# Kernel tuning notes

Hardware: AMD Instinct MI355X
Metric: run time of the kernel (lower is better)

Reference implementation:

```python
import jax, jax.numpy as jnp
import numpy as np

K, N, V_DIM, H_DIM, G_DIM, U_DIM = 8, 100000, 128, 128, 64, 128
W_SCALE = 0.1  # ~ xavier_uniform std for these fan-in/fan-out sizes


def setup_inputs() -> dict:
    key = jax.random.key(0)
    k1, k2, k3, k4, k5 = jax.random.split(key, 5)
    return {
        "vt": jax.random.normal(k1, (N, V_DIM), dtype=jnp.float32),
        "H": jax.random.normal(k2, (K, N, H_DIM), dtype=jnp.float32),
        "Wgv": jax.random.normal(k3, (V_DIM, G_DIM), dtype=jnp.float32) * W_SCALE,
        "Wgh": jax.random.normal(k4, (K, H_DIM, G_DIM), dtype=jnp.float32) * W_SCALE,
        "Wuh": jax.random.normal(k5, (K, H_DIM, U_DIM), dtype=jnp.float32) * W_SCALE,
    }


def reference(vt, H, Wgv, Wgh, Wuh):
    lrelu = lambda x: jnp.where(x >= 0, x, 0.01 * x)  # nn.LeakyReLU default slope
    g_key = vt @ Wgv                                   # [N, g]
    g_query = jnp.einsum("knh,khg->kng", H, Wgh)       # [k, N, g]
    g = jnp.einsum("kng,ng->kn", g_query, g_key)       # [k, N]
    g = jnp.exp(lrelu(g) / jnp.sqrt(jnp.float32(G_DIM)))
    beta = g / jnp.sum(g, axis=0, keepdims=True)       # normalize over k per node
    H_trans = jnp.einsum("knh,khu->knu", H, Wuh)       # [k, N, u]
    U = jnp.einsum("kn,knu->nu", beta, H_trans)        # [N, u]
    return lrelu(U)
```

## Files before the change

kernel.cpp:

```cpp
#include <hip/hip_runtime.h>
#include <stdint.h>

#define KH 8
#define HD 128
#define GD 64
#define UD 128
#define WPAD 136
#define NPB 64

typedef __attribute__((ext_vector_type(8))) short short8;
typedef __attribute__((ext_vector_type(4))) float f32x4;

__device__ __forceinline__ unsigned short f2bf(float x) {
    union { float f; unsigned u; } v; v.f = x;
    return (unsigned short)((v.u + 0x7fffu + ((v.u >> 16) & 1u)) >> 16);
}

__global__ void prep_weights(const float* __restrict__ Wgv,
                             const float* __restrict__ Wgh,
                             const float* __restrict__ Wuh,
                             unsigned short* __restrict__ ws) {
    const int wghN = KH * GD * WPAD;
    const int wuhN = KH * UD * WPAD;
    const int wgvN = GD * WPAD;
    int idx = blockIdx.x * 256 + threadIdx.x;
    if (idx >= wghN + wuhN + wgvN) return;
    float val = 0.f;
    if (idx < wghN) {
        int k = idx / (GD * WPAD), rem = idx % (GD * WPAD);
        int g = rem / WPAD, h = rem % WPAD;
        if (h < HD) val = Wgh[((size_t)k * HD + h) * GD + g];
    } else if (idx < wghN + wuhN) {
        int j = idx - wghN;
        int k = j / (UD * WPAD), rem = j % (UD * WPAD);
        int u = rem / WPAD, h = rem % WPAD;
        if (h < HD) val = Wuh[((size_t)k * HD + h) * UD + u];
    } else {
        int j = idx - wghN - wuhN;
        int g = j / WPAD, h = j % WPAD;
        if (h < HD) val = Wgv[(size_t)h * GD + g];
    }
    ws[idx] = f2bf(val);
}

__device__ __forceinline__ void cp_lds(const unsigned short* gs, unsigned short* ld,
                                       int nch, int wave, int lane) {
    for (int i = wave; i < nch; i += 4) {
        __builtin_amdgcn_global_load_lds(
            (const __attribute__((address_space(1))) unsigned int*)(gs + i * 512 + lane * 8),
            (__attribute__((address_space(3))) unsigned int*)(ld + i * 512),
            16, 0, 0);
    }
}

__launch_bounds__(256, 3)
__global__ void ghatt_main(const float* __restrict__ vt, const float* __restrict__ H,
                           const unsigned short* __restrict__ ws,
                           float* __restrict__ out, int N) {
    __shared__ unsigned short lds_h [NPB * WPAD];
    __shared__ unsigned short lds_wg[GD * WPAD];
    __shared__ unsigned short lds_wu[GD * WPAD];

    const int tid  = threadIdx.x;
    const int wave = tid >> 6;
    const int lane = tid & 63;
    const int cc   = lane & 15;
    const int q    = lane >> 4;
    const int nodebase = blockIdx.x * NPB;

    const unsigned short* wghT = ws;
    const unsigned short* wuhT = ws + (size_t)KH * GD * WPAD;
    const unsigned short* wgvT = ws + (size_t)KH * GD * WPAD + (size_t)KH * UD * WPAD;

    float4 hreg[8];

#pragma unroll
    for (int i = 0; i < 8; i++) {
        int f = tid + 256 * i, row = f >> 5, c4 = f & 31;
        int node = nodebase + row;
        float4 z; z.x = z.y = z.z = z.w = 0.f;
        float4 v = (node < N) ? ((const float4*)vt)[(size_t)node * 32 + c4] : z;
        short4 b;
        b.x = (short)f2bf(v.x); b.y = (short)f2bf(v.y);
        b.z = (short)f2bf(v.z); b.w = (short)f2bf(v.w);
        *(short4*)&lds_h[row * WPAD + c4 * 4] = b;
    }
    cp_lds(wgvT, lds_wg, 17, wave, lane);
    __syncthreads();

#pragma unroll
    for (int i = 0; i < 8; i++) {
        int f = tid + 256 * i, row = f >> 5, c4 = f & 31;
        int node = nodebase + row;
        float4 z; z.x = z.y = z.z = z.w = 0.f;
        hreg[i] = (node < N) ? ((const float4*)H)[(size_t)node * 32 + c4] : z;
    }

    f32x4 gkeyv[4];
    {
        short8 va[4];
#pragma unroll
        for (int kb = 0; kb < 4; kb++)
            va[kb] = *(const short8*)&lds_h[(wave * 16 + cc) * WPAD + kb * 32 + q * 8];
#pragma unroll
        for (int t = 0; t < 4; t++) {
            f32x4 acc = {0.f, 0.f, 0.f, 0.f};
#pragma unroll
            for (int kb = 0; kb < 4; kb++) {
                short8 vb = *(const short8*)&lds_wg[(t * 16 + cc) * WPAD + kb * 32 + q * 8];
                acc = __builtin_amdgcn_mfma_f32_16x16x32_bf16(va[kb], vb, acc, 0, 0, 0);
            }
            gkeyv[t] = acc;
        }
    }

    f32x4 Uacc[8];
#pragma unroll
    for (int t = 0; t < 8; t++) { Uacc[t].x = Uacc[t].y = Uacc[t].z = Uacc[t].w = 0.f; }
    float den[4] = {0.f, 0.f, 0.f, 0.f};

    for (int k = 0; k < KH; k++) {
        __syncthreads();
#pragma unroll
        for (int i = 0; i < 8; i++) {
            int f = tid + 256 * i, row = f >> 5, c4 = f & 31;
            short4 b;
            b.x = (short)f2bf(hreg[i].x); b.y = (short)f2bf(hreg[i].y);
            b.z = (short)f2bf(hreg[i].z); b.w = (short)f2bf(hreg[i].w);
            *(short4*)&lds_h[row * WPAD + c4 * 4] = b;
        }
        cp_lds(wghT + (size_t)k * (GD * WPAD), lds_wg, 17, wave, lane);
        cp_lds(wuhT + (size_t)k * (UD * WPAD), lds_wu, 17, wave, lane);
        __syncthreads();

        if (k < KH - 1) {
#pragma unroll
            for (int i = 0; i < 8; i++) {
                int f = tid + 256 * i, row = f >> 5, c4 = f & 31;
                int node = nodebase + row;
                float4 z; z.x = z.y = z.z = z.w = 0.f;
                hreg[i] = (node < N) ? ((const float4*)H)[((size_t)(k + 1) * N + node) * 32 + c4] : z;
            }
        }

        short8 va[4];
#pragma unroll
        for (int kb = 0; kb < 4; kb++)
            va[kb] = *(const short8*)&lds_h[(wave * 16 + cc) * WPAD + kb * 32 + q * 8];

        f32x4 gqv[4];
#pragma unroll
        for (int t = 0; t < 4; t++) {
            f32x4 acc = {0.f, 0.f, 0.f, 0.f};
#pragma unroll
            for (int kb = 0; kb < 4; kb++) {
                short8 vb = *(const short8*)&lds_wg[(t * 16 + cc) * WPAD + kb * 32 + q * 8];
                acc = __builtin_amdgcn_mfma_f32_16x16x32_bf16(va[kb], vb, acc, 0, 0, 0);
            }
            gqv[t] = acc;
        }

        float part[4];
#pragma unroll
        for (int r = 0; r < 4; r++)
            part[r] = gqv[0][r] * gkeyv[0][r] + gqv[1][r] * gkeyv[1][r]
                    + gqv[2][r] * gkeyv[2][r] + gqv[3][r] * gkeyv[3][r];
#pragma unroll
        for (int m2 = 1; m2 < 16; m2 <<= 1) {
#pragma unroll
            for (int r = 0; r < 4; r++) part[r] += __shfl_xor(part[r], m2);
        }
        float gg[4];
#pragma unroll
        for (int r = 0; r < 4; r++) {
            float x = part[r];
            x = (x >= 0.f) ? x : 0.01f * x;
            gg[r] = __expf(x * 0.125f);
            den[r] += gg[r];
        }

#pragma unroll
        for (int t = 0; t < 4; t++) {
            f32x4 acc = {0.f, 0.f, 0.f, 0.f};
#pragma unroll
            for (int kb = 0; kb < 4; kb++) {
                short8 vb = *(const short8*)&lds_wu[(t * 16 + cc) * WPAD + kb * 32 + q * 8];
                acc = __builtin_amdgcn_mfma_f32_16x16x32_bf16(va[kb], vb, acc, 0, 0, 0);
            }
#pragma unroll
            for (int r = 0; r < 4; r++) Uacc[t][r] += gg[r] * acc[r];
        }

        __syncthreads();
        cp_lds(wuhT + (size_t)k * (UD * WPAD) + (size_t)64 * WPAD, lds_wu, 17, wave, lane);
        __syncthreads();

#pragma unroll
        for (int t = 0; t < 4; t++) {
            f32x4 acc = {0.f, 0.f, 0.f, 0.f};
#pragma unroll
            for (int kb = 0; kb < 4; kb++) {
                short8 vb = *(const short8*)&lds_wu[(t * 16 + cc) * WPAD + kb * 32 + q * 8];
                acc = __builtin_amdgcn_mfma_f32_16x16x32_bf16(va[kb], vb, acc, 0, 0, 0);
            }
#pragma unroll
            for (int r = 0; r < 4; r++) Uacc[4 + t][r] += gg[r] * acc[r];
        }
    }

    float inv[4];
#pragma unroll
    for (int r = 0; r < 4; r++) inv[r] = 1.f / den[r];
#pragma unroll
    for (int t = 0; t < 8; t++) {
#pragma unroll
        for (int r = 0; r < 4; r++) {
            float u = Uacc[t][r] * inv[r];
            u = (u >= 0.f) ? u : 0.01f * u;
            int node = nodebase + wave * 16 + 4 * q + r;
            if (node < N) out[(size_t)node * UD + t * 16 + cc] = u;
        }
    }
}

extern "C" void kernel_launch(void* const* d_in, const int* in_sizes, int n_in,
                              void* d_out, int out_size, void* d_ws, size_t ws_size,
                              hipStream_t stream) {
    const float* vt  = (const float*)d_in[0];
    const float* H   = (const float*)d_in[1];
    const float* Wgv = (const float*)d_in[2];
    const float* Wgh = (const float*)d_in[3];
    const float* Wuh = (const float*)d_in[4];
    float* out = (float*)d_out;
    unsigned short* wsw = (unsigned short*)d_ws;

    const int N = in_sizes[0] / HD;

    const int prepTot = KH * GD * WPAD + KH * UD * WPAD + GD * WPAD;
    hipLaunchKernelGGL(prep_weights, dim3((prepTot + 255) / 256), dim3(256), 0, stream,
                       Wgv, Wgh, Wuh, wsw);

    hipLaunchKernelGGL(ghatt_main, dim3((N + NPB - 1) / NPB), dim3(256), 0, stream,
                       vt, H, wsw, out, N);
}
```

Before: 669.9 us.

## Drop LDS staging; load H rows and bf16 weights straight into MFMA registers

New measurement: 851.9 us. +27.2%, slower.

```diff
diff --git a/kernel.cpp b/kernel.cpp
--- a/kernel.cpp
+++ b/kernel.cpp
@@ -5,7 +5,6 @@
 #define HD 128
 #define GD 64
 #define UD 128
-#define WPAD 136
 #define NPB 64
 
 typedef __attribute__((ext_vector_type(8))) short short8;
@@ -20,151 +19,133 @@
                              const float* __restrict__ Wgh,
                              const float* __restrict__ Wuh,
                              unsigned short* __restrict__ ws) {
-    const int wghN = KH * GD * WPAD;
-    const int wuhN = KH * UD * WPAD;
-    const int wgvN = GD * WPAD;
+    const int wghN = KH * GD * HD;
+    const int wuhN = KH * UD * HD;
+    const int wgvN = GD * HD;
     int idx = blockIdx.x * 256 + threadIdx.x;
     if (idx >= wghN + wuhN + wgvN) return;
-    float val = 0.f;
+    float val;
     if (idx < wghN) {
-        int k = idx / (GD * WPAD), rem = idx % (GD * WPAD);
-        int g = rem / WPAD, h = rem % WPAD;
-        if (h < HD) val = Wgh[((size_t)k * HD + h) * GD + g];
+        int k = idx >> 13, rem = idx & 8191;
+        int g = rem >> 7, h = rem & 127;
+        val = Wgh[((size_t)k * HD + h) * GD + g];
     } else if (idx < wghN + wuhN) {
         int j = idx - wghN;
-        int k = j / (UD * WPAD), rem = j % (UD * WPAD);
-        int u = rem / WPAD, h = rem % WPAD;
-        if (h < HD) val = Wuh[((size_t)k * HD + h) * UD + u];
+        int k = j >> 14, rem = j & 16383;
+        int u = rem >> 7, h = rem & 127;
+        val = Wuh[((size_t)k * HD + h) * UD + u];
     } else {
         int j = idx - wghN - wuhN;
-        int g = j / WPAD, h = j % WPAD;
-        if (h < HD) val = Wgv[(size_t)h * GD + g];
+        int g = j >> 7, h = j & 127;
+        val = Wgv[(size_t)h * GD + g];
     }
     ws[idx] = f2bf(val);
-}
-
-__device__ __forceinline__ void cp_lds(const unsigned short* gs, unsigned short* ld,
-                                       int nch, int wave, int lane) {
-    for (int i = wave; i < nch; i += 4) {
-        __builtin_amdgcn_global_load_lds(
-            (const __attribute__((address_space(1))) unsigned int*)(gs + i * 512 + lane * 8),
-            (__attribute__((address_space(3))) unsigned int*)(ld + i * 512),
-            16, 0, 0);
-    }
 }
 
 __launch_bounds__(256, 3)
 __global__ void ghatt_main(const float* __restrict__ vt, const float* __restrict__ H,
                            const unsigned short* __restrict__ ws,
                            float* __restrict__ out, int N) {
-    __shared__ unsigned short lds_h [NPB * WPAD];
-    __shared__ unsigned short lds_wg[GD * WPAD];
-    __shared__ unsigned short lds_wu[GD * WPAD];
-
     const int tid  = threadIdx.x;
     const int wave = tid >> 6;
     const int lane = tid & 63;
     const int cc   = lane & 15;
     const int q    = lane >> 4;
-    const int nodebase = blockIdx.x * NPB;
+    const int nodebase = blockIdx.x * NPB + wave * 16;
+    const int node_a   = nodebase + cc;
+    const int nm       = node_a < N ? node_a : N - 1;
 
     const unsigned short* wghT = ws;
-    const unsigned short* wuhT = ws + (size_t)KH * GD * WPAD;
-    const unsigned short* wgvT = ws + (size_t)KH * GD * WPAD + (size_t)KH * UD * WPAD;
+    const unsigned short* wuhT = ws + (size_t)KH * GD * HD;
+    const unsigned short* wgvT = ws + (size_t)KH * GD * HD + (size_t)KH * UD * HD;
 
     float4 hreg[8];
-
-#pragma unroll
-    for (int i = 0; i < 8; i++) {
-        int f = tid + 256 * i, row = f >> 5, c4 = f & 31;
-        int node = nodebase + row;
-        float4 z; z.x = z.y = z.z = z.w = 0.f;
-        float4 v = (node < N) ? ((const float4*)vt)[(size_t)node * 32 + c4] : z;
-        short4 b;
-        b.x = (short)f2bf(v.x); b.y = (short)f2bf(v.y);
-        b.z = (short)f2bf(v.z); b.w = (short)f2bf(v.w);
-        *(short4*)&lds_h[row * WPAD + c4 * 4] = b;
-    }
-    cp_lds(wgvT, lds_wg, 17, wave, lane);
-    __syncthreads();
-
-#pragma unroll
-    for (int i = 0; i < 8; i++) {
-        int f = tid + 256 * i, row = f >> 5, c4 = f & 31;
-        int node = nodebase + row;
-        float4 z; z.x = z.y = z.z = z.w = 0.f;
-        hreg[i] = (node < N) ? ((const float4*)H)[(size_t)node * 32 + c4] : z;
-    }
-
-    f32x4 gkeyv[4];
+    short8 ha[4];
+
     {
-        short8 va[4];
-#pragma unroll
-        for (int kb = 0; kb < 4; kb++)
-            va[kb] = *(const short8*)&lds_h[(wave * 16 + cc) * WPAD + kb * 32 + q * 8];
+        const float* vrow = vt + (size_t)nm * HD + q * 8;
+#pragma unroll
+        for (int kb = 0; kb < 4; kb++) {
+            hreg[2 * kb]     = *(const float4*)(vrow + kb * 32);
+            hreg[2 * kb + 1] = *(const float4*)(vrow + kb * 32 + 4);
+        }
+#pragma unroll
+        for (int kb = 0; kb < 4; kb++) {
+            const float* p0 = (const float*)&hreg[2 * kb];
+            const float* p1 = (const float*)&hreg[2 * kb + 1];
+            short8 s;
+#pragma unroll
+            for (int j = 0; j < 4; j++) {
+                s[j]     = (short)f2bf(p0[j]);
+                s[4 + j] = (short)f2bf(p1[j]);
+            }
+            ha[kb] = s;
+        }
+    }
+    f32x4 gkey[4];
+#pragma unroll
+    for (int t = 0; t < 4; t++) {
+        f32x4 acc = {0.f, 0.f, 0.f, 0.f};
+#pragma unroll
+        for (int kb = 0; kb < 4; kb++) {
+            short8 wb = *(const short8*)(wgvT + (size_t)(t * 16 + cc) * HD + kb * 32 + q * 8);
+            acc = __builtin_amdgcn_mfma_f32_16x16x32_bf16(ha[kb], wb, acc, 0, 0, 0);
+        }
+        gkey[t] = acc;
+    }
+
+    f32x4 Uacc[8];
+#pragma unroll
+    for (int t = 0; t < 8; t++) { Uacc[t].x = Uacc[t].y = Uacc[t].z = Uacc[t].w = 0.f; }
+    float den[4] = {0.f, 0.f, 0.f, 0.f};
+
+    const float* hrow = H + (size_t)nm * HD + q * 8;
+#pragma unroll
+    for (int kb = 0; kb < 4; kb++) {
+        hreg[2 * kb]     = *(const float4*)(hrow + kb * 32);
+        hreg[2 * kb + 1] = *(const float4*)(hrow + kb * 32 + 4);
+    }
+
+    for (int k = 0; k < KH; k++) {
+#pragma unroll
+        for (int kb = 0; kb < 4; kb++) {
+            const float* p0 = (const float*)&hreg[2 * kb];
+            const float* p1 = (const float*)&hreg[2 * kb + 1];
+            short8 s;
+#pragma unroll
+            for (int j = 0; j < 4; j++) {
+                s[j]     = (short)f2bf(p0[j]);
+                s[4 + j] = (short)f2bf(p1[j]);
+            }
+            ha[kb] = s;
+        }
+        if (k < KH - 1) {
+            const float* hn = hrow + (size_t)(k + 1) * N * HD;
+#pragma unroll
+            for (int kb = 0; kb < 4; kb++) {
+                hreg[2 * kb]     = *(const float4*)(hn + kb * 32);
+                hreg[2 * kb + 1] = *(const float4*)(hn + kb * 32 + 4);
+            }
+        }
+
+        const unsigned short* wg = wghT + (size_t)k * GD * HD;
+        f32x4 gq[4];
 #pragma unroll
         for (int t = 0; t < 4; t++) {
             f32x4 acc = {0.f, 0.f, 0.f, 0.f};
 #pragma unroll
             for (int kb = 0; kb < 4; kb++) {
-                short8 vb = *(const short8*)&lds_wg[(t * 16 + cc) * WPAD + kb * 32 + q * 8];
-                acc = __builtin_amdgcn_mfma_f32_16x16x32_bf16(va[kb], vb, acc, 0, 0, 0);
-            }
-            gkeyv[t] = acc;
-        }
-    }
-
-    f32x4 Uacc[8];
-#pragma unroll
-    for (int t = 0; t < 8; t++) { Uacc[t].x = Uacc[t].y = Uacc[t].z = Uacc[t].w = 0.f; }
-    float den[4] = {0.f, 0.f, 0.f, 0.f};
-
-    for (int k = 0; k < KH; k++) {
-        __syncthreads();
-#pragma unroll
-        for (int i = 0; i < 8; i++) {
-            int f = tid + 256 * i, row = f >> 5, c4 = f & 31;
-            short4 b;
-            b.x = (short)f2bf(hreg[i].x); b.y = (short)f2bf(hreg[i].y);
-            b.z = (short)f2bf(hreg[i].z); b.w = (short)f2bf(hreg[i].w);
-            *(short4*)&lds_h[row * WPAD + c4 * 4] = b;
-        }
-        cp_lds(wghT + (size_t)k * (GD * WPAD), lds_wg, 17, wave, lane);
-        cp_lds(wuhT + (size_t)k * (UD * WPAD), lds_wu, 17, wave, lane);
-        __syncthreads();
-
-        if (k < KH - 1) {
-#pragma unroll
-            for (int i = 0; i < 8; i++) {
-                int f = tid + 256 * i, row = f >> 5, c4 = f & 31;
-                int node = nodebase + row;
-                float4 z; z.x = z.y = z.z = z.w = 0.f;
-                hreg[i] = (node < N) ? ((const float4*)H)[((size_t)(k + 1) * N + node) * 32 + c4] : z;
-            }
-        }
-
-        short8 va[4];
-#pragma unroll
-        for (int kb = 0; kb < 4; kb++)
-            va[kb] = *(const short8*)&lds_h[(wave * 16 + cc) * WPAD + kb * 32 + q * 8];
-
-        f32x4 gqv[4];
-#pragma unroll
-        for (int t = 0; t < 4; t++) {
-            f32x4 acc = {0.f, 0.f, 0.f, 0.f};
-#pragma unroll
-            for (int kb = 0; kb < 4; kb++) {
-                short8 vb = *(const short8*)&lds_wg[(t * 16 + cc) * WPAD + kb * 32 + q * 8];
-                acc = __builtin_amdgcn_mfma_f32_16x16x32_bf16(va[kb], vb, acc, 0, 0, 0);
-            }
-            gqv[t] = acc;
+                short8 wb = *(const short8*)(wg + (size_t)(t * 16 + cc) * HD + kb * 32 + q * 8);
+                acc = __builtin_amdgcn_mfma_f32_16x16x32_bf16(ha[kb], wb, acc, 0, 0, 0);
+            }
+            gq[t] = acc;
         }
 
         float part[4];
 #pragma unroll
         for (int r = 0; r < 4; r++)
-            part[r] = gqv[0][r] * gkeyv[0][r] + gqv[1][r] * gkeyv[1][r]
-                    + gqv[2][r] * gkeyv[2][r] + gqv[3][r] * gkeyv[3][r];
+            part[r] = gq[0][r] * gkey[0][r] + gq[1][r] * gkey[1][r]
+                    + gq[2][r] * gkey[2][r] + gq[3][r] * gkey[3][r];
 #pragma unroll
         for (int m2 = 1; m2 < 16; m2 <<= 1) {
 #pragma unroll
@@ -179,32 +160,17 @@
             den[r] += gg[r];
         }
 
-#pragma unroll
-        for (int t = 0; t < 4; t++) {
+        const unsigned short* wu = wuhT + (size_t)k * UD * HD;
+#pragma unroll
+        for (int t = 0; t < 8; t++) {
             f32x4 acc = {0.f, 0.f, 0.f, 0.f};
 #pragma unroll
             for (int kb = 0; kb < 4; kb++) {
-                short8 vb = *(const short8*)&lds_wu[(t * 16 + cc) * WPAD + kb * 32 + q * 8];
-                acc = __builtin_amdgcn_mfma_f32_16x16x32_bf16(va[kb], vb, acc, 0, 0, 0);
+                short8 wb = *(const short8*)(wu + (size_t)(t * 16 + cc) * HD + kb * 32 + q * 8);
+                acc = __builtin_amdgcn_mfma_f32_16x16x32_bf16(ha[kb], wb, acc, 0, 0, 0);
             }
 #pragma unroll
             for (int r = 0; r < 4; r++) Uacc[t][r] += gg[r] * acc[r];
-        }
-
-        __syncthreads();
-        cp_lds(wuhT + (size_t)k * (UD * WPAD) + (size_t)64 * WPAD, lds_wu, 17, wave, lane);
-        __syncthreads();
-
-#pragma unroll
-        for (int t = 0; t < 4; t++) {
-            f32x4 acc = {0.f, 0.f, 0.f, 0.f};
-#pragma unroll
-            for (int kb = 0; kb < 4; kb++) {
-                short8 vb = *(const short8*)&lds_wu[(t * 16 + cc) * WPAD + kb * 32 + q * 8];
-                acc = __builtin_amdgcn_mfma_f32_16x16x32_bf16(va[kb], vb, acc, 0, 0, 0);
-            }
-#pragma unroll
-            for (int r = 0; r < 4; r++) Uacc[4 + t][r] += gg[r] * acc[r];
         }
     }
 
@@ -217,7 +183,7 @@
         for (int r = 0; r < 4; r++) {
             float u = Uacc[t][r] * inv[r];
             u = (u >= 0.f) ? u : 0.01f * u;
-            int node = nodebase + wave * 16 + 4 * q + r;
+            int node = nodebase + 4 * q + r;
             if (node < N) out[(size_t)node * UD + t * 16 + cc] = u;
         }
     }
@@ -236,7 +202,7 @@
 
     const int N = in_sizes[0] / HD;
 
-    const int prepTot = KH * GD * WPAD + KH * UD * WPAD + GD * WPAD;
+    const int prepTot = KH * GD * HD + KH * UD * HD + GD * HD;
     hipLaunchKernelGGL(prep_weights, dim3((prepTot + 255) / 256), dim3(256), 0, stream,
                        Wgv, Wgh, Wuh, wsw);
 
```
